# Kernel tuning notes

Measured on AMD Instinct MI355X. Metric: run time of the kernel, lower is better.

The kernel has to match this reference:

```python
import jax, jax.numpy as jnp
import numpy as np

B, K = 16, 64          # batch, n_particles
IN = 128               # sensory input dim
H0, H1 = 192, 64       # wiring layer sizes (H0+H1 = state_size 256)
UNF = 6                # ode_unfolds
EPS = 1e-8
BK = B * K


def _layer_params(key, n_in, h, sigma_init=0.1):
    ks = jax.random.split(key, 11)
    u = lambda k, sh, lo, hi: jax.random.uniform(k, sh, dtype=jnp.float32) * (hi - lo) + lo
    return dict(
        gleak=u(ks[0], (h,), 0.001, 1.0),
        vleak=u(ks[1], (h,), -0.2, 0.2),
        cm=u(ks[2], (h,), 0.4, 0.6),
        iw=u(ks[3], (n_in, h), 0.001, 1.0),
        isig=u(ks[4], (n_in, h), 3.0, 8.0),
        imu=u(ks[5], (n_in, h), 0.3, 0.8),
        ierev=jax.random.normal(ks[6], (n_in, h), dtype=jnp.float32),
        w=u(ks[7], (h, h), 0.001, 1.0),
        sig=u(ks[8], (h, h), 3.0, 8.0),
        mu=u(ks[9], (h, h), 0.3, 0.8),
        erev=jax.random.normal(ks[10], (h, h), dtype=jnp.float32),
        gdiff=jnp.full((h,), sigma_init, dtype=jnp.float32),
    )


def setup_inputs() -> dict:
    key = jax.random.key(0)
    k = jax.random.split(key, 6)
    inp = {
        'x': jax.random.normal(k[0], (B, IN), dtype=jnp.float32),
        'particles': jax.random.normal(k[1], (B, K, H0 + H1), dtype=jnp.float32) * 0.1,
        'log_weights': jnp.full((B, K), -np.log(K), dtype=jnp.float32),
        'noise0': jax.random.normal(k[2], (UNF, BK, H0), dtype=jnp.float32),
        'noise1': jax.random.normal(k[3], (UNF, BK, H1), dtype=jnp.float32),
    }
    p0 = _layer_params(k[4], IN, H0)
    p1 = _layer_params(k[5], H0, H1)
    for n, v in p0.items():
        inp[n + '0'] = v
    for n, v in p1.items():
        inp[n + '1'] = v
    return inp


def _drift(v, x, gleak, vleak, cm, iw, isig, imu, ierev, w, sig, mu, erev):
    # x: [BK, n_in], v: [BK, h]
    ia = jax.nn.relu(iw) * jax.nn.sigmoid(isig * (x[:, :, None] - imu))   # [BK, n_in, h]
    w_num_in = jnp.einsum('bih,ih->bh', ia, ierev)
    w_den_in = ia.sum(axis=1)
    wa = jax.nn.relu(w) * jax.nn.sigmoid(sig * (v[:, :, None] - mu))      # [BK, h, h]
    w_num = jnp.einsum('bih,ih->bh', wa, erev) + w_num_in
    w_den = wa.sum(axis=1) + w_den_in
    gl = jax.nn.relu(gleak)
    c = jax.nn.relu(cm) + EPS
    return (gl * vleak + w_num - (gl + w_den) * v) / c


def _unfold(v0, x, noise, gdiff, dt, drift_params):
    sdt = jnp.sqrt(dt)
    def step(v, n):
        d = _drift(v, x, *drift_params)
        return v + d * dt + gdiff * sdt * n, None
    v, _ = jax.lax.scan(step, v0, noise)
    return v


def reference(x, particles, log_weights, noise0, noise1,
              gleak0, vleak0, cm0, iw0, isig0, imu0, ierev0, w0, sig0, mu0, erev0, gdiff0,
              gleak1, vleak1, cm1, iw1, isig1, imu1, ierev1, w1, sig1, mu1, erev1, gdiff1):
    dt = jnp.float32(1.0 / UNF)  # elapsed=1.0 split over n_unfolds
    xk = jnp.broadcast_to(x[:, None, :], (B, K, IN)).reshape(BK, IN)
    v0 = particles[..., :H0].reshape(BK, H0)
    v1 = particles[..., H0:].reshape(BK, H1)
    p0 = (gleak0, vleak0, cm0, iw0, isig0, imu0, ierev0, w0, sig0, mu0, erev0)
    p1 = (gleak1, vleak1, cm1, iw1, isig1, imu1, ierev1, w1, sig1, mu1, erev1)
    s0 = _unfold(v0, xk, noise0, gdiff0, dt, p0)      # layer 0 output feeds layer 1
    s1 = _unfold(v1, s0, noise1, gdiff1, dt, p1)
    new_particles = jnp.concatenate([s0.reshape(B, K, H0), s1.reshape(B, K, H1)], axis=-1)
    # uniform weights -> ESS = K, resampler is a no-op; output = weighted particle mean
    wts = jax.nn.softmax(log_weights, axis=1)[..., None]   # [B, K, 1]
    output = (wts * s1.reshape(B, K, H1)).sum(axis=1)      # [B, H1]
    return output, new_particles, log_weights
```

## Files before the change

### kernel.cpp

```cpp
#include <hip/hip_runtime.h>
#include <math.h>

constexpr int B   = 16;
constexpr int K   = 64;
constexpr int BK  = B * K;
constexpr int IN  = 128;
constexpr int H0  = 192;
constexpr int H1  = 64;
constexpr int UNF = 6;
constexpr float EPS = 1e-8f;
constexpr float DT  = 1.0f / 6.0f;
constexpr float L2E = 1.4426950408889634f;

static __device__ __forceinline__ float rcpf(float x) {
    return __builtin_amdgcn_rcpf(x);
}
static __device__ __forceinline__ float exp2_fast(float x) {
#if __has_builtin(__builtin_amdgcn_exp2f)
    return __builtin_amdgcn_exp2f(x);
#else
    return exp2f(x);
#endif
}
static __device__ __forceinline__ float sig_from_t(float t) {
    return rcpf(1.0f + exp2_fast(t));
}

constexpr int NPACK    = H0 * H0 + H0 * H1 + H1 * H1;
constexpr int NPACKBLK = NPACK / 256;
__global__ __launch_bounds__(256) void prep_kernel(
    const float* __restrict__ w0,  const float* __restrict__ sig0,
    const float* __restrict__ mu0, const float* __restrict__ erev0,
    const float* __restrict__ iw1, const float* __restrict__ isig1,
    const float* __restrict__ imu1,const float* __restrict__ ierev1,
    const float* __restrict__ w1,  const float* __restrict__ sig1,
    const float* __restrict__ mu1, const float* __restrict__ erev1,
    const float* __restrict__ x,   const float* __restrict__ iw0,
    const float* __restrict__ isig0,const float* __restrict__ imu0,
    const float* __restrict__ ierev0,
    float4* __restrict__ pack0, float4* __restrict__ packi1,
    float4* __restrict__ pack1,
    float* __restrict__ in_num, float* __restrict__ in_den)
{
    __shared__ float xs[IN];
    if (blockIdx.x < NPACKBLK) {
        const int t = blockIdx.x * 256 + threadIdx.x;
        constexpr int N0 = H0 * H0;
        constexpr int N1 = H0 * H1;
        if (t < N0) {
            const float wv = fmaxf(w0[t], 0.0f);
            pack0[t] = make_float4(wv, sig0[t] * L2E, sig0[t] * mu0[t] * L2E,
                                   wv * erev0[t]);
        } else if (t < N0 + N1) {
            const int u = t - N0;
            const float wv = fmaxf(iw1[u], 0.0f);
            packi1[u] = make_float4(wv, isig1[u] * L2E,
                                    isig1[u] * imu1[u] * L2E, wv * ierev1[u]);
        } else {
            const int u = t - N0 - N1;
            const float wv = fmaxf(w1[u], 0.0f);
            pack1[u] = make_float4(wv, sig1[u] * L2E, sig1[u] * mu1[u] * L2E,
                                   wv * erev1[u]);
        }
    } else {
        const int b = blockIdx.x - NPACKBLK;
        const int h = threadIdx.x;
        if (h < IN) xs[h] = x[b * IN + h];
        __syncthreads();
        if (h < H0) {
            float num = 0.0f, den = 0.0f;
            #pragma unroll 4
            for (int i = 0; i < IN; ++i) {
                const int idx = i * H0 + h;
                const float wv = fmaxf(iw0[idx], 0.0f);
                const float t  = isig0[idx] * L2E * (imu0[idx] - xs[i]);
                const float a  = wv * sig_from_t(t);
                num = fmaf(a, ierev0[idx], num);
                den += a;
            }
            in_num[b * H0 + h] = num;
            in_den[b * H0 + h] = den;
        }
    }
}

__global__ __launch_bounds__(768) void fused_unfold_kernel(
    const float* __restrict__ particles,
    const float* __restrict__ noise0,
    const float* __restrict__ noise1,
    const float* __restrict__ gleak0, const float* __restrict__ vleak0,
    const float* __restrict__ cm0,    const float* __restrict__ gdiff0,
    const float* __restrict__ gleak1, const float* __restrict__ vleak1,
    const float* __restrict__ cm1,    const float* __restrict__ gdiff1,
    const float4* __restrict__ pack0,
    const float4* __restrict__ packi1,
    const float4* __restrict__ pack1,
    const float* __restrict__ in_num,
    const float* __restrict__ in_den,
    float* __restrict__ outp)
{
    const int tid = threadIdx.x;
    const int h   = tid % H0;
    const int q   = tid / H0;
    const int bk0 = blockIdx.x * 4;
    const int b   = blockIdx.x >> 4;

    __shared__ __align__(16) float vs[H0][4];
    __shared__ float2 part0[4][4][H0];
    __shared__ __align__(16) float v1s[H1][4];
    __shared__ float2 part1[8][4][H1];

    vs[h][q] = particles[(bk0 + q) * 256 + h];
    float nz[UNF];
    #pragma unroll
    for (int s = 0; s < UNF; ++s)
        nz[s] = noise0[s * (BK * H0) + (bk0 + q) * H0 + h];

    const float gl    = fmaxf(gleak0[h], 0.0f);
    const float glvl  = gl * vleak0[h];
    const float cinv  = rcpf(fmaxf(cm0[h], 0.0f) + EPS);
    const float gd    = gdiff0[h] * sqrtf(DT);
    const float innum = in_num[b * H0 + h];
    const float inden = in_den[b * H0 + h];
    __syncthreads();

    const int ibase = 48 * q;
    for (int step = 0; step < UNF; ++step) {
        float num[4] = {0.f, 0.f, 0.f, 0.f};
        float den[4] = {0.f, 0.f, 0.f, 0.f};
        #pragma unroll 4
        for (int ii = 0; ii < 48; ++ii) {
            const int i = ibase + ii;
            const float4 p  = pack0[i * H0 + h];
            const float4 vv = *(const float4*)&vs[i][0];
            #pragma unroll
            for (int m = 0; m < 4; ++m) {
                const float v = (m == 0) ? vv.x : (m == 1) ? vv.y
                              : (m == 2) ? vv.z : vv.w;
                const float s = sig_from_t(fmaf(-p.y, v, p.z));
                num[m] = fmaf(s, p.w, num[m]);
                den[m] = fmaf(s, p.x, den[m]);
            }
        }
        #pragma unroll
        for (int m = 0; m < 4; ++m)
            part0[q][m][h] = make_float2(num[m], den[m]);
        __syncthreads();
        float tn = innum, td = inden;
        #pragma unroll
        for (int j = 0; j < 4; ++j) {
            const float2 t = part0[j][q][h];
            tn += t.x; td += t.y;
        }
        const float vh = vs[h][q];
        const float d  = (glvl + tn - (gl + td) * vh) * cinv;
        vs[h][q] = fmaf(gd, nz[step], fmaf(d, DT, vh));
        __syncthreads();
    }

    outp[(bk0 + q) * 256 + h] = vs[h][q];

    const int h1 = tid & 63;
    const int qq = tid >> 6;
    float nz1[UNF];
    if (tid < 256) {
        v1s[h1][qq] = particles[(bk0 + qq) * 256 + H0 + h1];
        #pragma unroll
        for (int s = 0; s < UNF; ++s)
            nz1[s] = noise1[s * (BK * H1) + (bk0 + qq) * H1 + h1];
    }

    float gl1 = 0.f, glvl1 = 0.f, cinv1 = 0.f, gd1 = 0.f;
    float in1n[4] = {0.f, 0.f, 0.f, 0.f};
    float in1d[4] = {0.f, 0.f, 0.f, 0.f};
    if (tid < 512) {
        gl1   = fmaxf(gleak1[h1], 0.0f);
        glvl1 = gl1 * vleak1[h1];
        cinv1 = rcpf(fmaxf(cm1[h1], 0.0f) + EPS);
        gd1   = gdiff1[h1] * sqrtf(DT);
        #pragma unroll 4
        for (int ii = 0; ii < 24; ++ii) {
            const int i = qq * 24 + ii;
            const float4 p  = packi1[i * H1 + h1];
            const float4 vv = *(const float4*)&vs[i][0];
            #pragma unroll
            for (int m = 0; m < 4; ++m) {
                const float v = (m == 0) ? vv.x : (m == 1) ? vv.y
                              : (m == 2) ? vv.z : vv.w;
                const float s = sig_from_t(fmaf(-p.y, v, p.z));
                in1n[m] = fmaf(s, p.w, in1n[m]);
                in1d[m] = fmaf(s, p.x, in1d[m]);
            }
        }
    }
    __syncthreads();

    for (int step = 0; step < UNF; ++step) {
        if (tid < 512) {
            float num[4], den[4];
            #pragma unroll
            for (int m = 0; m < 4; ++m) { num[m] = in1n[m]; den[m] = in1d[m]; }
            #pragma unroll
            for (int ii = 0; ii < 8; ++ii) {
                const int i = qq * 8 + ii;
                const float4 p  = pack1[i * H1 + h1];
                const float4 vv = *(const float4*)&v1s[i][0];
                #pragma unroll
                for (int m = 0; m < 4; ++m) {
                    const float v = (m == 0) ? vv.x : (m == 1) ? vv.y
                                  : (m == 2) ? vv.z : vv.w;
                    const float s = sig_from_t(fmaf(-p.y, v, p.z));
                    num[m] = fmaf(s, p.w, num[m]);
                    den[m] = fmaf(s, p.x, den[m]);
                }
            }
            #pragma unroll
            for (int m = 0; m < 4; ++m)
                part1[qq][m][h1] = make_float2(num[m], den[m]);
        }
        __syncthreads();
        if (tid < 256) {
            float tn = 0.f, td = 0.f;
            #pragma unroll
            for (int j = 0; j < 8; ++j) {
                const float2 t = part1[j][qq][h1];
                tn += t.x; td += t.y;
            }
            const float vh = v1s[h1][qq];
            const float d  = (glvl1 + tn - (gl1 + td) * vh) * cinv1;
            v1s[h1][qq] = fmaf(gd1, nz1[step], fmaf(d, DT, vh));
        }
        __syncthreads();
    }

    if (tid < 256)
        outp[(bk0 + qq) * 256 + H0 + h1] = v1s[h1][qq];
}

__global__ __launch_bounds__(64) void finalize_kernel(
    const float* __restrict__ log_weights,
    const float* __restrict__ newp,
    float* __restrict__ out_y,
    float* __restrict__ out_lw)
{
    const int t = threadIdx.x;
    const int b = blockIdx.x;

    const float lw = log_weights[b * K + t];
    out_lw[b * K + t] = lw;

    float mx = lw;
    #pragma unroll
    for (int o = 32; o > 0; o >>= 1) mx = fmaxf(mx, __shfl_xor(mx, o));
    const float e = __expf(lw - mx);
    float s = e;
    #pragma unroll
    for (int o = 32; o > 0; o >>= 1) s += __shfl_xor(s, o);

    __shared__ float wk[K];
    wk[t] = e / s;
    __syncthreads();

    float acc = 0.0f;
    for (int k = 0; k < K; ++k)
        acc = fmaf(wk[k], newp[(b * K + k) * 256 + H0 + t], acc);
    out_y[b * H1 + t] = acc;
}

extern "C" void kernel_launch(void* const* d_in, const int* in_sizes, int n_in,
                              void* d_out, int out_size, void* d_ws, size_t ws_size,
                              hipStream_t stream) {
    const float* x           = (const float*)d_in[0];
    const float* particles   = (const float*)d_in[1];
    const float* log_weights = (const float*)d_in[2];
    const float* noise0      = (const float*)d_in[3];
    const float* noise1      = (const float*)d_in[4];
    const float* gleak0 = (const float*)d_in[5];
    const float* vleak0 = (const float*)d_in[6];
    const float* cm0    = (const float*)d_in[7];
    const float* iw0    = (const float*)d_in[8];
    const float* isig0  = (const float*)d_in[9];
    const float* imu0   = (const float*)d_in[10];
    const float* ierev0 = (const float*)d_in[11];
    const float* w0     = (const float*)d_in[12];
    const float* sig0   = (const float*)d_in[13];
    const float* mu0    = (const float*)d_in[14];
    const float* erev0  = (const float*)d_in[15];
    const float* gdiff0 = (const float*)d_in[16];
    const float* gleak1 = (const float*)d_in[17];
    const float* vleak1 = (const float*)d_in[18];
    const float* cm1    = (const float*)d_in[19];
    const float* iw1    = (const float*)d_in[20];
    const float* isig1  = (const float*)d_in[21];
    const float* imu1   = (const float*)d_in[22];
    const float* ierev1 = (const float*)d_in[23];
    const float* w1     = (const float*)d_in[24];
    const float* sig1   = (const float*)d_in[25];
    const float* mu1    = (const float*)d_in[26];
    const float* erev1  = (const float*)d_in[27];
    const float* gdiff1 = (const float*)d_in[28];

    float* out    = (float*)d_out;
    float* out_y  = out;
    float* out_np = out + B * H1;
    float* out_lw = out + B * H1 + BK * 256;

    float* ws      = (float*)d_ws;
    float4* pack0  = (float4*)(ws);
    float4* packi1 = (float4*)(ws + 4 * 36864);
    float4* pack1  = (float4*)(ws + 4 * (36864 + 12288));
    float*  in_num0 = ws + 4 * (36864 + 12288 + 4096);
    float*  in_den0 = in_num0 + B * H0;

    prep_kernel<<<NPACKBLK + B, 256, 0, stream>>>(
        w0, sig0, mu0, erev0, iw1, isig1, imu1, ierev1, w1, sig1, mu1, erev1,
        x, iw0, isig0, imu0, ierev0,
        pack0, packi1, pack1, in_num0, in_den0);

    fused_unfold_kernel<<<BK / 4, 768, 0, stream>>>(
        particles, noise0, noise1,
        gleak0, vleak0, cm0, gdiff0,
        gleak1, vleak1, cm1, gdiff1,
        pack0, packi1, pack1, in_num0, in_den0, out_np);

    finalize_kernel<<<B, 64, 0, stream>>>(log_weights, out_np, out_y, out_lw);
}
```

Before: 205.9 us.

## Fuse finalize into unfold kernel, widen block to 960 threads for layer-0 sweep

Removes the separate finalize kernel: softmax weights are computed inside the unfold block and the weighted mean is accumulated into out_y with atomicAdd, after a memset. The block grows to 960 threads so the layer-0 reduction over 192 inputs is split five ways (40,40,40,40,32) instead of four ways of 48. The layer-1 noise and state loads are hoisted to the kernel start, and the inner loops are manually unrolled. This trades a kernel launch and a global re-read for atomics and a memset, and it raises register pressure because of the larger block.

Result: faster. 195.2 us (-5.2%).

```diff
diff --git a/kernel.cpp b/kernel.cpp
--- a/kernel.cpp
+++ b/kernel.cpp
@@ -84,10 +84,33 @@
     }
 }
 
-__global__ __launch_bounds__(768) void fused_unfold_kernel(
+template <int LEN>
+static __device__ __forceinline__ void sweep0_body(
+    const float4* __restrict__ pp,
+    const float* vsbase, int ibase,
+    float num[4], float den[4])
+{
+    #pragma unroll 8
+    for (int ii = 0; ii < LEN; ++ii) {
+        const float4 p  = pp[(size_t)ii * H0];
+        const float4 vv = *(const float4*)(vsbase + (ibase + ii) * 4);
+        float s;
+        s = sig_from_t(fmaf(-p.y, vv.x, p.z));
+        num[0] = fmaf(s, p.w, num[0]); den[0] = fmaf(s, p.x, den[0]);
+        s = sig_from_t(fmaf(-p.y, vv.y, p.z));
+        num[1] = fmaf(s, p.w, num[1]); den[1] = fmaf(s, p.x, den[1]);
+        s = sig_from_t(fmaf(-p.y, vv.z, p.z));
+        num[2] = fmaf(s, p.w, num[2]); den[2] = fmaf(s, p.x, den[2]);
+        s = sig_from_t(fmaf(-p.y, vv.w, p.z));
+        num[3] = fmaf(s, p.w, num[3]); den[3] = fmaf(s, p.x, den[3]);
+    }
+}
+
+__global__ __launch_bounds__(960) void fused_unfold_kernel(
     const float* __restrict__ particles,
     const float* __restrict__ noise0,
     const float* __restrict__ noise1,
+    const float* __restrict__ log_weights,
     const float* __restrict__ gleak0, const float* __restrict__ vleak0,
     const float* __restrict__ cm0,    const float* __restrict__ gdiff0,
     const float* __restrict__ gleak1, const float* __restrict__ vleak1,
@@ -97,24 +120,54 @@
     const float4* __restrict__ pack1,
     const float* __restrict__ in_num,
     const float* __restrict__ in_den,
-    float* __restrict__ outp)
+    float* __restrict__ outp,
+    float* __restrict__ out_y,
+    float* __restrict__ out_lw)
 {
     const int tid = threadIdx.x;
     const int h   = tid % H0;
     const int q   = tid / H0;
     const int bk0 = blockIdx.x * 4;
     const int b   = blockIdx.x >> 4;
+    const int k0  = (blockIdx.x & 15) * 4;
+
+    const int h1  = tid & 63;
+    const int qq  = tid >> 6;
 
     __shared__ __align__(16) float vs[H0][4];
-    __shared__ float2 part0[4][4][H0];
+    __shared__ float2 part0[5][4][H0];
     __shared__ __align__(16) float v1s[H1][4];
     __shared__ float2 part1[8][4][H1];
-
-    vs[h][q] = particles[(bk0 + q) * 256 + h];
+    __shared__ float  w4[4];
+
+    if (tid < 64) {
+        const float lw = log_weights[b * K + tid];
+        out_lw[b * K + tid] = lw;
+        float mx = lw;
+        #pragma unroll
+        for (int o = 32; o > 0; o >>= 1) mx = fmaxf(mx, __shfl_xor(mx, o));
+        const float e = __expf(lw - mx);
+        float ssum = e;
+        #pragma unroll
+        for (int o = 32; o > 0; o >>= 1) ssum += __shfl_xor(ssum, o);
+        if (tid >= k0 && tid < k0 + 4) w4[tid - k0] = e / ssum;
+    }
+
+    float nz1[UNF];
+    if (tid < 256) {
+        v1s[h1][qq] = particles[(bk0 + qq) * 256 + H0 + h1];
+        #pragma unroll
+        for (int s = 0; s < UNF; ++s)
+            nz1[s] = noise1[s * (BK * H1) + (bk0 + qq) * H1 + h1];
+    }
+
     float nz[UNF];
-    #pragma unroll
-    for (int s = 0; s < UNF; ++s)
-        nz[s] = noise0[s * (BK * H0) + (bk0 + q) * H0 + h];
+    if (q < 4) {
+        vs[h][q] = particles[(bk0 + q) * 256 + h];
+        #pragma unroll
+        for (int s = 0; s < UNF; ++s)
+            nz[s] = noise0[s * (BK * H0) + (bk0 + q) * H0 + h];
+    }
 
     const float gl    = fmaxf(gleak0[h], 0.0f);
     const float glvl  = gl * vleak0[h];
@@ -124,51 +177,32 @@
     const float inden = in_den[b * H0 + h];
     __syncthreads();
 
-    const int ibase = 48 * q;
+    const int ibase = (q == 4) ? 160 : 40 * q;
+    const float4* pp = pack0 + (size_t)ibase * H0 + h;
     for (int step = 0; step < UNF; ++step) {
         float num[4] = {0.f, 0.f, 0.f, 0.f};
         float den[4] = {0.f, 0.f, 0.f, 0.f};
-        #pragma unroll 4
-        for (int ii = 0; ii < 48; ++ii) {
-            const int i = ibase + ii;
-            const float4 p  = pack0[i * H0 + h];
-            const float4 vv = *(const float4*)&vs[i][0];
-            #pragma unroll
-            for (int m = 0; m < 4; ++m) {
-                const float v = (m == 0) ? vv.x : (m == 1) ? vv.y
-                              : (m == 2) ? vv.z : vv.w;
-                const float s = sig_from_t(fmaf(-p.y, v, p.z));
-                num[m] = fmaf(s, p.w, num[m]);
-                den[m] = fmaf(s, p.x, den[m]);
-            }
-        }
+        if (q == 4) sweep0_body<32>(pp, &vs[0][0], ibase, num, den);
+        else        sweep0_body<40>(pp, &vs[0][0], ibase, num, den);
         #pragma unroll
         for (int m = 0; m < 4; ++m)
             part0[q][m][h] = make_float2(num[m], den[m]);
         __syncthreads();
-        float tn = innum, td = inden;
-        #pragma unroll
-        for (int j = 0; j < 4; ++j) {
-            const float2 t = part0[j][q][h];
-            tn += t.x; td += t.y;
-        }
-        const float vh = vs[h][q];
-        const float d  = (glvl + tn - (gl + td) * vh) * cinv;
-        vs[h][q] = fmaf(gd, nz[step], fmaf(d, DT, vh));
-        __syncthreads();
-    }
-
-    outp[(bk0 + q) * 256 + h] = vs[h][q];
-
-    const int h1 = tid & 63;
-    const int qq = tid >> 6;
-    float nz1[UNF];
-    if (tid < 256) {
-        v1s[h1][qq] = particles[(bk0 + qq) * 256 + H0 + h1];
-        #pragma unroll
-        for (int s = 0; s < UNF; ++s)
-            nz1[s] = noise1[s * (BK * H1) + (bk0 + qq) * H1 + h1];
-    }
+        if (q < 4) {
+            float tn = innum, td = inden;
+            #pragma unroll
+            for (int j = 0; j < 5; ++j) {
+                const float2 t = part0[j][q][h];
+                tn += t.x; td += t.y;
+            }
+            const float vh = vs[h][q];
+            const float d  = (glvl + tn - (gl + td) * vh) * cinv;
+            vs[h][q] = fmaf(gd, nz[step], fmaf(d, DT, vh));
+        }
+        __syncthreads();
+    }
+
+    if (q < 4) outp[(bk0 + q) * 256 + h] = vs[h][q];
 
     float gl1 = 0.f, glvl1 = 0.f, cinv1 = 0.f, gd1 = 0.f;
     float in1n[4] = {0.f, 0.f, 0.f, 0.f};
@@ -183,14 +217,15 @@
             const int i = qq * 24 + ii;
             const float4 p  = packi1[i * H1 + h1];
             const float4 vv = *(const float4*)&vs[i][0];
-            #pragma unroll
-            for (int m = 0; m < 4; ++m) {
-                const float v = (m == 0) ? vv.x : (m == 1) ? vv.y
-                              : (m == 2) ? vv.z : vv.w;
-                const float s = sig_from_t(fmaf(-p.y, v, p.z));
-                in1n[m] = fmaf(s, p.w, in1n[m]);
-                in1d[m] = fmaf(s, p.x, in1d[m]);
-            }
+            float s;
+            s = sig_from_t(fmaf(-p.y, vv.x, p.z));
+            in1n[0] = fmaf(s, p.w, in1n[0]); in1d[0] = fmaf(s, p.x, in1d[0]);
+            s = sig_from_t(fmaf(-p.y, vv.y, p.z));
+            in1n[1] = fmaf(s, p.w, in1n[1]); in1d[1] = fmaf(s, p.x, in1d[1]);
+            s = sig_from_t(fmaf(-p.y, vv.z, p.z));
+            in1n[2] = fmaf(s, p.w, in1n[2]); in1d[2] = fmaf(s, p.x, in1d[2]);
+            s = sig_from_t(fmaf(-p.y, vv.w, p.z));
+            in1n[3] = fmaf(s, p.w, in1n[3]); in1d[3] = fmaf(s, p.x, in1d[3]);
         }
     }
     __syncthreads();
@@ -205,14 +240,15 @@
                 const int i = qq * 8 + ii;
                 const float4 p  = pack1[i * H1 + h1];
                 const float4 vv = *(const float4*)&v1s[i][0];
-                #pragma unroll
-                for (int m = 0; m < 4; ++m) {
-                    const float v = (m == 0) ? vv.x : (m == 1) ? vv.y
-                                  : (m == 2) ? vv.z : vv.w;
-                    const float s = sig_from_t(fmaf(-p.y, v, p.z));
-                    num[m] = fmaf(s, p.w, num[m]);
-                    den[m] = fmaf(s, p.x, den[m]);
-                }
+                float s;
+                s = sig_from_t(fmaf(-p.y, vv.x, p.z));
+                num[0] = fmaf(s, p.w, num[0]); den[0] = fmaf(s, p.x, den[0]);
+                s = sig_from_t(fmaf(-p.y, vv.y, p.z));
+                num[1] = fmaf(s, p.w, num[1]); den[1] = fmaf(s, p.x, den[1]);
+                s = sig_from_t(fmaf(-p.y, vv.z, p.z));
+                num[2] = fmaf(s, p.w, num[2]); den[2] = fmaf(s, p.x, den[2]);
+                s = sig_from_t(fmaf(-p.y, vv.w, p.z));
+                num[3] = fmaf(s, p.w, num[3]); den[3] = fmaf(s, p.x, den[3]);
             }
             #pragma unroll
             for (int m = 0; m < 4; ++m)
@@ -235,36 +271,12 @@
 
     if (tid < 256)
         outp[(bk0 + qq) * 256 + H0 + h1] = v1s[h1][qq];
-}
-
-__global__ __launch_bounds__(64) void finalize_kernel(
-    const float* __restrict__ log_weights,
-    const float* __restrict__ newp,
-    float* __restrict__ out_y,
-    float* __restrict__ out_lw)
-{
-    const int t = threadIdx.x;
-    const int b = blockIdx.x;
-
-    const float lw = log_weights[b * K + t];
-    out_lw[b * K + t] = lw;
-
-    float mx = lw;
-    #pragma unroll
-    for (int o = 32; o > 0; o >>= 1) mx = fmaxf(mx, __shfl_xor(mx, o));
-    const float e = __expf(lw - mx);
-    float s = e;
-    #pragma unroll
-    for (int o = 32; o > 0; o >>= 1) s += __shfl_xor(s, o);
-
-    __shared__ float wk[K];
-    wk[t] = e / s;
-    __syncthreads();
-
-    float acc = 0.0f;
-    for (int k = 0; k < K; ++k)
-        acc = fmaf(wk[k], newp[(b * K + k) * 256 + H0 + t], acc);
-    out_y[b * H1 + t] = acc;
+
+    if (tid < 64) {
+        const float acc = w4[0] * v1s[tid][0] + w4[1] * v1s[tid][1]
+                        + w4[2] * v1s[tid][2] + w4[3] * v1s[tid][3];
+        atomicAdd(&out_y[b * H1 + tid], acc);
+    }
 }
 
 extern "C" void kernel_launch(void* const* d_in, const int* in_sizes, int n_in,
@@ -312,16 +324,17 @@
     float*  in_num0 = ws + 4 * (36864 + 12288 + 4096);
     float*  in_den0 = in_num0 + B * H0;
 
+    hipMemsetAsync(out_y, 0, B * H1 * sizeof(float), stream);
+
     prep_kernel<<<NPACKBLK + B, 256, 0, stream>>>(
         w0, sig0, mu0, erev0, iw1, isig1, imu1, ierev1, w1, sig1, mu1, erev1,
         x, iw0, isig0, imu0, ierev0,
         pack0, packi1, pack1, in_num0, in_den0);
 
-    fused_unfold_kernel<<<BK / 4, 768, 0, stream>>>(
-        particles, noise0, noise1,
+    fused_unfold_kernel<<<BK / 4, 960, 0, stream>>>(
+        particles, noise0, noise1, log_weights,
         gleak0, vleak0, cm0, gdiff0,
         gleak1, vleak1, cm1, gdiff1,
-        pack0, packi1, pack1, in_num0, in_den0, out_np);
-
-    finalize_kernel<<<B, 64, 0, stream>>>(log_weights, out_np, out_y, out_lw);
-}
+        pack0, packi1, pack1, in_num0, in_den0,
+        out_np, out_y, out_lw);
+}
```
